# Performance work log

Hardware: AMD Instinct MI355X
Metric: run time of the kernel (lower is better)

Reference implementation:

```python
import jax, jax.numpy as jnp
import numpy as np


def setup_inputs() -> dict:
    key = jax.random.key(0)
    k1, k2, k3 = jax.random.split(key, 3)
    T, B, D, H = 256, 64, 1024, 2048
    sigma = 0.01
    inputs = jax.random.normal(k1, (T, B, D), dtype=jnp.float32)
    state = jnp.zeros((B, H), dtype=jnp.float32)
    W_xh = jax.random.uniform(k2, (D, H), dtype=jnp.float32) * sigma
    W_hh = jax.random.uniform(k3, (H, H), dtype=jnp.float32) * sigma
    b_h = jnp.zeros((H,), dtype=jnp.float32)
    return {"inputs": inputs, "state": state, "W_xh": W_xh, "W_hh": W_hh, "b_h": b_h}


def reference(inputs, state, W_xh, W_hh, b_h):
    # Precompute input projection for all steps in one big GEMM: [T,B,H]
    x_proj = jnp.einsum('tbd,dh->tbh', inputs, W_xh) + b_h

    def step(h, xp):
        h = jnp.tanh(h @ W_hh + xp)
        return h, h

    final_state, outputs = jax.lax.scan(step, state, x_proj)
    # outputs: [T, B, H] (stacked per-step hidden states), final_state: [B, H]
    return outputs, final_state
```

## Files before the change

### kernel.cpp

```cpp
#include <hip/hip_runtime.h>
#include <hip/hip_bf16.h>

#define T_STEPS 256
#define B_SZ    64
#define D_SZ    1024
#define H_SZ    2048
#define NBLK    256
#define TPB     320
#define HBUF    (B_SZ * H_SZ)

#define W_SCALE     256.0f
#define W_INV_SCALE 0.00390625f

typedef __attribute__((ext_vector_type(8))) _Float16 f16x8;
typedef __attribute__((ext_vector_type(4))) float    f32x4;


__global__ void cvt_f32_f16(const float* __restrict__ in,
                            _Float16* __restrict__ out, int n, float scale) {
    int i = blockIdx.x * blockDim.x + threadIdx.x;
    if (i < n) out[i] = (_Float16)(in[i] * scale);
}

__global__ void transpose_to_f16(const float* __restrict__ in,
                                 _Float16* __restrict__ out,
                                 int rows, int log2cols, float scale) {
    int i = blockIdx.x * blockDim.x + threadIdx.x;
    int cols = 1 << log2cols;
    if (i >= rows * cols) return;
    int r = i >> log2cols;
    int c = i & (cols - 1);
    out[c * rows + r] = (_Float16)(in[i] * scale);
}

__global__ void init_ctrs(unsigned int* ctr) {
    ctr[threadIdx.x + blockIdx.x * blockDim.x] = 0u;
}

__global__ __launch_bounds__(256) void gemm_xproj(
    const _Float16* __restrict__ A,
    const _Float16* __restrict__ BT,
    const float* __restrict__ bias,
    float* __restrict__ C,
    int M, int N, int K)
{
    int wave = threadIdx.x >> 6;
    int lane = threadIdx.x & 63;
    int q = lane >> 4;
    int r = lane & 15;
    int m0 = blockIdx.x * 128 + (wave >> 1) * 64;
    int n0 = blockIdx.y * 128 + (wave & 1) * 64;

    f32x4 acc[4][4] = {};
    for (int k = 0; k < K; k += 32) {
        int kk = k + q * 8;
        f16x8 a[4], b[4];
#pragma unroll
        for (int i = 0; i < 4; i++)
            a[i] = *(const f16x8*)(A + (size_t)(m0 + i * 16 + r) * K + kk);
#pragma unroll
        for (int j = 0; j < 4; j++)
            b[j] = *(const f16x8*)(BT + (size_t)(n0 + j * 16 + r) * K + kk);
#pragma unroll
        for (int i = 0; i < 4; i++)
#pragma unroll
            for (int j = 0; j < 4; j++)
                acc[i][j] = __builtin_amdgcn_mfma_f32_16x16x32_f16(a[i], b[j], acc[i][j], 0, 0, 0);
    }
#pragma unroll
    for (int i = 0; i < 4; i++)
#pragma unroll
        for (int j = 0; j < 4; j++)
#pragma unroll
            for (int reg = 0; reg < 4; reg++) {
                int row = m0 + i * 16 + q * 4 + reg;
                int col = n0 + j * 16 + r;
                C[(size_t)row * N + col] = acc[i][j][reg] * W_INV_SCALE + bias[col];
            }
}

template<bool CHAIN>
__global__ __launch_bounds__(TPB, 1) void rnn_persist(
    _Float16* __restrict__ hbase,
    _Float16* __restrict__ hb1,
    const _Float16* __restrict__ WT,
    float* __restrict__ out,
    float* __restrict__ final_out,
    unsigned int* __restrict__ ctr)
{
    __shared__ f16x8 wfrag[8192];
    __shared__ float part[4][2][256];
    __shared__ __align__(16) _Float16 hsl[16 * 32];
    __shared__ int pdone[4];
    __shared__ int hdone1, go;

    int tid = threadIdx.x;
    int bid = blockIdx.x;
    int g   = (bid >> 1) & 3;
    int c   = ((bid >> 3) << 1) | (bid & 1);
    int n0  = c * 32;
    int row0 = g * 16;

    if (tid == 0) {
        pdone[0] = pdone[1] = pdone[2] = pdone[3] = 0;
        hdone1 = 0; go = 0;
    }

    for (int idx = tid; idx < 8192; idx += TPB) {
        int kb = idx >> 7, j = (idx >> 6) & 1, l = idx & 63;
        wfrag[idx] = *(const f16x8*)(WT + (size_t)(n0 + j * 16 + (l & 15)) * H_SZ
                                        + kb * 32 + (l >> 4) * 8);
    }
    __syncthreads();

    int wave = tid >> 6, lane = tid & 63;

    if (wave == 4) {
        float c0 = 1.0f + lane, c1 = 2.0f, c2 = 3.0f, c3 = 4.0f;
        const float k1 = 1.0000001f, k2 = 1.0e-30f;
        while (__hip_atomic_load(&go, __ATOMIC_RELAXED, __HIP_MEMORY_SCOPE_WORKGROUP) < T_STEPS) {
#pragma unroll
            for (int z = 0; z < 64; z++) {
                c0 = __builtin_fmaf(c0, k1, k2);
                c1 = __builtin_fmaf(c1, k1, k2);
                c2 = __builtin_fmaf(c2, k1, k2);
                c3 = __builtin_fmaf(c3, k1, k2);
            }
        }
        __asm__ volatile("" :: "v"(c0), "v"(c1), "v"(c2), "v"(c3));
        return;
    }

    int q = lane >> 4, r = lane & 15;
    unsigned int* aline = ctr + (g * 2 + (bid & 1)) * 32;

    float xp[4];
    if (wave < 2) {
#pragma unroll
        for (int s = 0; s < 4; s++)
            xp[s] = out[(size_t)(row0 + q + 4 * s) * H_SZ + n0 + wave * 16 + r];
    }

    for (int t = 0; t < T_STEPS; t++) {
        const _Float16* hp;
        _Float16*       hn;
        if constexpr (CHAIN) {
            hp = hbase + (size_t)t * HBUF;
            hn = hbase + (size_t)(t + 1) * HBUF;
        } else {
            hp = (t & 1) ? hb1 : hbase;
            hn = (t & 1) ? hbase : hb1;
        }
        float* out_t = out + (size_t)t * B_SZ * H_SZ;
        int tg = t + 1;

        const _Float16* arow = hp + (size_t)(row0 + r) * H_SZ + q * 8;
        f16x8 abuf[16];
#pragma unroll
        for (int p = 0; p < 16; p++) {
            if constexpr (CHAIN) {
                abuf[p] = *(const f16x8*)(arow + (wave * 16 + p) * 32);
            } else {
                union { unsigned long long u[2]; f16x8 v; } au;
                au.u[0] = __hip_atomic_load((unsigned long long*)(arow + (wave * 16 + p) * 32),
                                            __ATOMIC_RELAXED, __HIP_MEMORY_SCOPE_AGENT);
                au.u[1] = __hip_atomic_load((unsigned long long*)(arow + (wave * 16 + p) * 32) + 1,
                                            __ATOMIC_RELAXED, __HIP_MEMORY_SCOPE_AGENT);
                abuf[p] = au.v;
            }
        }
        f32x4 acc[2] = {};
#pragma unroll
        for (int p = 0; p < 16; p++) {
            int kb = wave * 16 + p;
            acc[0] = __builtin_amdgcn_mfma_f32_16x16x32_f16(abuf[p], wfrag[kb * 128 + lane],      acc[0], 0, 0, 0);
            acc[1] = __builtin_amdgcn_mfma_f32_16x16x32_f16(abuf[p], wfrag[kb * 128 + 64 + lane], acc[1], 0, 0, 0);
        }

#pragma unroll
        for (int h = 0; h < 2; h++)
            *(f32x4*)&part[wave][h][lane * 4] = acc[h];
        __asm__ volatile("s_waitcnt lgkmcnt(0)" ::: "memory");
        if (lane == 0)
            __hip_atomic_store(&pdone[wave], tg, __ATOMIC_RELAXED, __HIP_MEMORY_SCOPE_WORKGROUP);

        if (wave >= 2) {
            if (t == T_STEPS - 1) break;
            while (__hip_atomic_load(&go, __ATOMIC_RELAXED, __HIP_MEMORY_SCOPE_WORKGROUP) < tg) { }
            continue;
        }

        for (int w = 0; w < 4; w++)
            if (w != wave)
                while (__hip_atomic_load(&pdone[w], __ATOMIC_RELAXED, __HIP_MEMORY_SCOPE_WORKGROUP) < tg) { }
        __asm__ volatile("" ::: "memory");

        bool last = (t == T_STEPS - 1);
#pragma unroll
        for (int s = 0; s < 4; s++) {
            int row = q + 4 * s;
            int idx = (s * 16 + r) * 4 + q;
            float sum = part[0][wave][idx] + part[1][wave][idx]
                      + part[2][wave][idx] + part[3][wave][idx];
            float v = tanhf(sum * W_INV_SCALE + xp[s]);
            size_t o = (size_t)(row0 + row) * H_SZ + n0 + wave * 16 + r;
            out_t[o] = v;
            if (last) final_out[o] = v;
            hsl[row * 32 + wave * 16 + r] = (_Float16)v;
        }
        if (last) {
            if (wave == 0 && lane == 0)
                __hip_atomic_store(&go, T_STEPS, __ATOMIC_RELAXED, __HIP_MEMORY_SCOPE_WORKGROUP);
            break;
        }

        const float* out_t1 = out_t + B_SZ * H_SZ;
#pragma unroll
        for (int s = 0; s < 4; s++)
            xp[s] = out_t1[(size_t)(row0 + q + 4 * s) * H_SZ + n0 + wave * 16 + r];

        __asm__ volatile("s_waitcnt lgkmcnt(0)" ::: "memory");
        {
            int rl = lane >> 2, pi = wave * 4 + (lane & 3);
            unsigned long long vv = ((const unsigned long long*)hsl)[rl * 8 + pi];
            __hip_atomic_store((unsigned long long*)(hn + (size_t)(row0 + rl) * H_SZ + n0) + pi,
                               vv, __ATOMIC_RELAXED, __HIP_MEMORY_SCOPE_AGENT);
        }
        __builtin_amdgcn_s_waitcnt(0);

        if (wave == 1) {
            if (lane == 0)
                __hip_atomic_store(&hdone1, tg, __ATOMIC_RELAXED, __HIP_MEMORY_SCOPE_WORKGROUP);
            while (__hip_atomic_load(&go, __ATOMIC_RELAXED, __HIP_MEMORY_SCOPE_WORKGROUP) < tg) { }
            continue;
        }
        while (__hip_atomic_load(&hdone1, __ATOMIC_RELAXED, __HIP_MEMORY_SCOPE_WORKGROUP) < tg) { }
        if (lane == 0)
            __hip_atomic_fetch_add(aline, 1u, __ATOMIC_RELAXED, __HIP_MEMORY_SCOPE_AGENT);
        unsigned int line_tgt = (unsigned int)tg * 32u;
        for (;;) {
            unsigned int v = __hip_atomic_load(ctr + (g * 2 + (lane & 1)) * 32,
                                               __ATOMIC_RELAXED, __HIP_MEMORY_SCOPE_AGENT);
            if (__ballot(v < line_tgt) == 0ull) break;
        }
        if (lane == 0)
            __hip_atomic_store(&go, tg, __ATOMIC_RELAXED, __HIP_MEMORY_SCOPE_WORKGROUP);
    }
}


extern "C" void kernel_launch(void* const* d_in, const int* in_sizes, int n_in,
                              void* d_out, int out_size, void* d_ws, size_t ws_size,
                              hipStream_t stream) {
    const float* inputs = (const float*)d_in[0];
    const float* state  = (const float*)d_in[1];
    const float* W_xh   = (const float*)d_in[2];
    const float* W_hh   = (const float*)d_in[3];
    const float* b_h    = (const float*)d_in[4];
    float* out = (float*)d_out;
    char* ws = (char*)d_ws;

    const size_t MB = 1ull << 20;
    const size_t OFF_WXT   = 0;
    const size_t OFF_WHT   = 4 * MB;
    const size_t OFF_CTR   = 12 * MB;
    const size_t OFF_CHAIN = 12 * MB + 8192;
    const size_t NEED_CHAIN = OFF_CHAIN + (size_t)(T_STEPS + 1) * HBUF * 2;

    const size_t F_IN  = 0;
    const size_t F_WXT = F_IN  + (size_t)T_STEPS * B_SZ * D_SZ * 2;
    const size_t F_WHT = F_WXT + (size_t)H_SZ * D_SZ * 2;
    const size_t F_H0  = F_WHT + (size_t)H_SZ * H_SZ * 2;
    const size_t F_H1  = F_H0  + (size_t)HBUF * 2;
    const size_t F_CTR = F_H1  + (size_t)HBUF * 2;
    const size_t NEED_PP = F_CTR + 4096;

    const int n_in_el = T_STEPS * B_SZ * D_SZ;
    dim3 g1((T_STEPS * B_SZ) / 128, H_SZ / 128);
    float* final_out = out + (size_t)T_STEPS * B_SZ * H_SZ;

    if (ws_size >= NEED_CHAIN) {
        _Float16* WxT    = (_Float16*)(ws + OFF_WXT);
        _Float16* WhT    = (_Float16*)(ws + OFF_WHT);
        unsigned int* ctr = (unsigned int*)(ws + OFF_CTR);
        _Float16* hchain = (_Float16*)(ws + OFF_CHAIN);
        _Float16* inputs_f16 = hchain + HBUF;
        _Float16* hb1 = nullptr;

        cvt_f32_f16<<<(n_in_el + 255) / 256, 256, 0, stream>>>(inputs, inputs_f16, n_in_el, 1.0f);
        transpose_to_f16<<<(D_SZ * H_SZ + 255) / 256, 256, 0, stream>>>(W_xh, WxT, D_SZ, 11, W_SCALE);
        transpose_to_f16<<<(H_SZ * H_SZ + 255) / 256, 256, 0, stream>>>(W_hh, WhT, H_SZ, 11, W_SCALE);
        cvt_f32_f16<<<(B_SZ * H_SZ + 255) / 256, 256, 0, stream>>>(state, hchain, B_SZ * H_SZ, 1.0f);
        init_ctrs<<<4, 256, 0, stream>>>(ctr);

        gemm_xproj<<<g1, 256, 0, stream>>>(inputs_f16, WxT, b_h, out,
                                           T_STEPS * B_SZ, H_SZ, D_SZ);

        void* args[] = { (void*)&hchain, (void*)&hb1, (void*)&WhT,
                         (void*)&out, (void*)&final_out, (void*)&ctr };
        hipLaunchCooperativeKernel((void*)rnn_persist<true>, dim3(NBLK), dim3(TPB),
                                   args, 0, stream);
    } else {
        if (ws_size < NEED_PP) return;
        _Float16* inputs_f16 = (_Float16*)(ws + F_IN);
        _Float16* WxT    = (_Float16*)(ws + F_WXT);
        _Float16* WhT    = (_Float16*)(ws + F_WHT);
        _Float16* hbuf0  = (_Float16*)(ws + F_H0);
        _Float16* hbuf1  = (_Float16*)(ws + F_H1);
        unsigned int* ctr = (unsigned int*)(ws + F_CTR);

        cvt_f32_f16<<<(n_in_el + 255) / 256, 256, 0, stream>>>(inputs, inputs_f16, n_in_el, 1.0f);
        transpose_to_f16<<<(D_SZ * H_SZ + 255) / 256, 256, 0, stream>>>(W_xh, WxT, D_SZ, 11, W_SCALE);
        transpose_to_f16<<<(H_SZ * H_SZ + 255) / 256, 256, 0, stream>>>(W_hh, WhT, H_SZ, 11, W_SCALE);
        cvt_f32_f16<<<(B_SZ * H_SZ + 255) / 256, 256, 0, stream>>>(state, hbuf0, B_SZ * H_SZ, 1.0f);
        init_ctrs<<<4, 256, 0, stream>>>(ctr);

        gemm_xproj<<<g1, 256, 0, stream>>>(inputs_f16, WxT, b_h, out,
                                           T_STEPS * B_SZ, H_SZ, D_SZ);

        void* args[] = { (void*)&hbuf0, (void*)&hbuf1, (void*)&WhT,
                         (void*)&out, (void*)&final_out, (void*)&ctr };
        hipLaunchCooperativeKernel((void*)rnn_persist<false>, dim3(NBLK), dim3(TPB),
                                   args, 0, stream);
    }
}
```

Before: 1.816 ms.

## Fuse input projection into persistent RNN kernel via a producer wave

Adds a sixth wave per block that computes each step's input projection slice with MFMA directly from fp16 inputs and W_xh. It writes the slice into double-buffered shared memory, and the tanh waves wait on a flag for it. This removes the separate large x-projection GEMM and its fp32 round trip through the output buffer, overlapping that work with the recurrence. The conversion kernels are also vectorised, and the weight transposes now use a shared-memory tile for coalescing. The cost is that the producer wave's global loads can add latency to the serial step chain if it falls behind.

```diff
diff --git a/kernel.cpp b/kernel.cpp
--- a/kernel.cpp
+++ b/kernel.cpp
@@ -6,31 +6,42 @@
 #define D_SZ    1024
 #define H_SZ    2048
 #define NBLK    256
-#define TPB     320
+#define TPB_F   384
+#define TPB_NF  320
 #define HBUF    (B_SZ * H_SZ)
 
 #define W_SCALE     256.0f
 #define W_INV_SCALE 0.00390625f
 
 typedef __attribute__((ext_vector_type(8))) _Float16 f16x8;
+typedef __attribute__((ext_vector_type(4))) _Float16 f16x4;
 typedef __attribute__((ext_vector_type(4))) float    f32x4;
 
 
 __global__ void cvt_f32_f16(const float* __restrict__ in,
-                            _Float16* __restrict__ out, int n, float scale) {
+                            _Float16* __restrict__ out, int n4, float scale) {
     int i = blockIdx.x * blockDim.x + threadIdx.x;
-    if (i < n) out[i] = (_Float16)(in[i] * scale);
+    if (i < n4) {
+        float4 v = ((const float4*)in)[i];
+        f16x4 o = { (_Float16)(v.x * scale), (_Float16)(v.y * scale),
+                    (_Float16)(v.z * scale), (_Float16)(v.w * scale) };
+        ((f16x4*)out)[i] = o;
+    }
 }
 
 __global__ void transpose_to_f16(const float* __restrict__ in,
                                  _Float16* __restrict__ out,
-                                 int rows, int log2cols, float scale) {
-    int i = blockIdx.x * blockDim.x + threadIdx.x;
-    int cols = 1 << log2cols;
-    if (i >= rows * cols) return;
-    int r = i >> log2cols;
-    int c = i & (cols - 1);
-    out[c * rows + r] = (_Float16)(in[i] * scale);
+                                 int rows, int cols, float scale) {
+    __shared__ float tile[32][33];
+    int tx = threadIdx.x & 31, ty = threadIdx.x >> 5;
+    int r0 = blockIdx.y * 32, c0 = blockIdx.x * 32;
+#pragma unroll
+    for (int i = 0; i < 32; i += 8)
+        tile[ty + i][tx] = in[(size_t)(r0 + ty + i) * cols + c0 + tx];
+    __syncthreads();
+#pragma unroll
+    for (int i = 0; i < 32; i += 8)
+        out[(size_t)(c0 + ty + i) * rows + r0 + tx] = (_Float16)(tile[tx][ty + i] * scale);
 }
 
 __global__ void init_ctrs(unsigned int* ctr) {
@@ -79,20 +90,25 @@
             }
 }
 
-template<bool CHAIN>
-__global__ __launch_bounds__(TPB, 1) void rnn_persist(
+template<bool CHAIN, bool FUSED>
+__global__ __launch_bounds__(TPB_F, 1) void rnn_persist(
     _Float16* __restrict__ hbase,
     _Float16* __restrict__ hb1,
     const _Float16* __restrict__ WT,
+    const _Float16* __restrict__ xin,
+    const _Float16* __restrict__ WxT,
+    const float*    __restrict__ bias,
     float* __restrict__ out,
     float* __restrict__ final_out,
     unsigned int* __restrict__ ctr)
 {
+    constexpr int NT = FUSED ? TPB_F : TPB_NF;
     __shared__ f16x8 wfrag[8192];
     __shared__ float part[4][2][256];
     __shared__ __align__(16) _Float16 hsl[16 * 32];
+    __shared__ float xpl[2][16][32];
     __shared__ int pdone[4];
-    __shared__ int hdone1, go;
+    __shared__ int hdone1, go, xpready;
 
     int tid = threadIdx.x;
     int bid = blockIdx.x;
@@ -103,10 +119,10 @@
 
     if (tid == 0) {
         pdone[0] = pdone[1] = pdone[2] = pdone[3] = 0;
-        hdone1 = 0; go = 0;
-    }
-
-    for (int idx = tid; idx < 8192; idx += TPB) {
+        hdone1 = 0; go = 0; xpready = 0;
+    }
+
+    for (int idx = tid; idx < 8192; idx += NT) {
         int kb = idx >> 7, j = (idx >> 6) & 1, l = idx & 63;
         wfrag[idx] = *(const f16x8*)(WT + (size_t)(n0 + j * 16 + (l & 15)) * H_SZ
                                         + kb * 32 + (l >> 4) * 8);
@@ -131,14 +147,56 @@
         return;
     }
 
+    if constexpr (FUSED) {
+        if (wave == 5) {
+            int q = lane >> 4, r = lane & 15;
+            float bj0 = bias[n0 + r];
+            float bj1 = bias[n0 + 16 + r];
+            const _Float16* wr0 = WxT + (size_t)(n0 + r) * D_SZ + q * 8;
+            const _Float16* wr1 = WxT + (size_t)(n0 + 16 + r) * D_SZ + q * 8;
+            for (int t = 0; t < T_STEPS; t++) {
+                if (t >= 2)
+                    while (__hip_atomic_load(&go, __ATOMIC_RELAXED, __HIP_MEMORY_SCOPE_WORKGROUP) < t - 1) { }
+                const _Float16* xr = xin + ((size_t)t * B_SZ + row0 + r) * D_SZ + q * 8;
+                f32x4 xacc0 = {}, xacc1 = {};
+                for (int k = 0; k < D_SZ; k += 128) {
+                    f16x8 xa[4], xb0[4], xb1[4];
+#pragma unroll
+                    for (int p = 0; p < 4; p++) {
+                        xa[p]  = *(const f16x8*)(xr  + k + p * 32);
+                        xb0[p] = *(const f16x8*)(wr0 + k + p * 32);
+                        xb1[p] = *(const f16x8*)(wr1 + k + p * 32);
+                    }
+#pragma unroll
+                    for (int p = 0; p < 4; p++) {
+                        xacc0 = __builtin_amdgcn_mfma_f32_16x16x32_f16(xa[p], xb0[p], xacc0, 0, 0, 0);
+                        xacc1 = __builtin_amdgcn_mfma_f32_16x16x32_f16(xa[p], xb1[p], xacc1, 0, 0, 0);
+                    }
+                }
+                float* xs = &xpl[t & 1][0][0];
+#pragma unroll
+                for (int reg = 0; reg < 4; reg++) {
+                    xs[(q * 4 + reg) * 32 + r]      = xacc0[reg] * W_INV_SCALE + bj0;
+                    xs[(q * 4 + reg) * 32 + 16 + r] = xacc1[reg] * W_INV_SCALE + bj1;
+                }
+                __asm__ volatile("s_waitcnt lgkmcnt(0)" ::: "memory");
+                if (lane == 0)
+                    __hip_atomic_store(&xpready, t + 1, __ATOMIC_RELAXED, __HIP_MEMORY_SCOPE_WORKGROUP);
+            }
+            return;
+        }
+    }
+
     int q = lane >> 4, r = lane & 15;
     unsigned int* aline = ctr + (g * 2 + (bid & 1)) * 32;
 
-    float xp[4];
-    if (wave < 2) {
-#pragma unroll
-        for (int s = 0; s < 4; s++)
-            xp[s] = out[(size_t)(row0 + q + 4 * s) * H_SZ + n0 + wave * 16 + r];
+    float xp[4] = {0.f, 0.f, 0.f, 0.f};
+    if constexpr (!FUSED) {
+        if (wave < 2) {
+#pragma unroll
+            for (int s = 0; s < 4; s++)
+                xp[s] = out[(size_t)(row0 + q + 4 * s) * H_SZ + n0 + wave * 16 + r];
+        }
     }
 
     for (int t = 0; t < T_STEPS; t++) {
@@ -195,6 +253,11 @@
                 while (__hip_atomic_load(&pdone[w], __ATOMIC_RELAXED, __HIP_MEMORY_SCOPE_WORKGROUP) < tg) { }
         __asm__ volatile("" ::: "memory");
 
+        if constexpr (FUSED) {
+            while (__hip_atomic_load(&xpready, __ATOMIC_RELAXED, __HIP_MEMORY_SCOPE_WORKGROUP) < tg) { }
+            __asm__ volatile("" ::: "memory");
+        }
+
         bool last = (t == T_STEPS - 1);
 #pragma unroll
         for (int s = 0; s < 4; s++) {
@@ -202,7 +265,10 @@
             int idx = (s * 16 + r) * 4 + q;
             float sum = part[0][wave][idx] + part[1][wave][idx]
                       + part[2][wave][idx] + part[3][wave][idx];
-            float v = tanhf(sum * W_INV_SCALE + xp[s]);
+            float xv;
+            if constexpr (FUSED) xv = xpl[t & 1][row][wave * 16 + r];
+            else                 xv = xp[s];
+            float v = tanhf(sum * W_INV_SCALE + xv);
             size_t o = (size_t)(row0 + row) * H_SZ + n0 + wave * 16 + r;
             out_t[o] = v;
             if (last) final_out[o] = v;
@@ -214,10 +280,12 @@
             break;
         }
 
-        const float* out_t1 = out_t + B_SZ * H_SZ;
-#pragma unroll
-        for (int s = 0; s < 4; s++)
-            xp[s] = out_t1[(size_t)(row0 + q + 4 * s) * H_SZ + n0 + wave * 16 + r];
+        if constexpr (!FUSED) {
+            const float* out_t1 = out_t + B_SZ * H_SZ;
+#pragma unroll
+            for (int s = 0; s < 4; s++)
+                xp[s] = out_t1[(size_t)(row0 + q + 4 * s) * H_SZ + n0 + wave * 16 + r];
+        }
 
         __asm__ volatile("s_waitcnt lgkmcnt(0)" ::: "memory");
         {
@@ -261,14 +329,20 @@
     char* ws = (char*)d_ws;
 
     const size_t MB = 1ull << 20;
-    const size_t OFF_WXT   = 0;
-    const size_t OFF_WHT   = 4 * MB;
-    const size_t OFF_CTR   = 12 * MB;
-    const size_t OFF_CHAIN = 12 * MB + 8192;
+    const size_t XIN_BYTES = (size_t)T_STEPS * B_SZ * D_SZ * 2;
+
+    const size_t OFF_WXT     = 0;
+    const size_t OFF_WHT     = 4 * MB;
+    const size_t OFF_CTR     = 12 * MB;
+    const size_t OFF_XIN     = 12 * MB + 8192;
+    const size_t OFF_CHAIN_F = OFF_XIN + XIN_BYTES;
+    const size_t NEED_FUSED  = OFF_CHAIN_F + (size_t)(T_STEPS + 1) * HBUF * 2;
+
+    const size_t OFF_CHAIN  = 12 * MB + 8192;
     const size_t NEED_CHAIN = OFF_CHAIN + (size_t)(T_STEPS + 1) * HBUF * 2;
 
     const size_t F_IN  = 0;
-    const size_t F_WXT = F_IN  + (size_t)T_STEPS * B_SZ * D_SZ * 2;
+    const size_t F_WXT = F_IN  + XIN_BYTES;
     const size_t F_WHT = F_WXT + (size_t)H_SZ * D_SZ * 2;
     const size_t F_H0  = F_WHT + (size_t)H_SZ * H_SZ * 2;
     const size_t F_H1  = F_H0  + (size_t)HBUF * 2;
@@ -279,26 +353,54 @@
     dim3 g1((T_STEPS * B_SZ) / 128, H_SZ / 128);
     float* final_out = out + (size_t)T_STEPS * B_SZ * H_SZ;
 
-    if (ws_size >= NEED_CHAIN) {
-        _Float16* WxT    = (_Float16*)(ws + OFF_WXT);
-        _Float16* WhT    = (_Float16*)(ws + OFF_WHT);
+    if (ws_size >= NEED_FUSED) {
+        _Float16* WxT     = (_Float16*)(ws + OFF_WXT);
+        _Float16* WhT     = (_Float16*)(ws + OFF_WHT);
         unsigned int* ctr = (unsigned int*)(ws + OFF_CTR);
-        _Float16* hchain = (_Float16*)(ws + OFF_CHAIN);
+        _Float16* xin     = (_Float16*)(ws + OFF_XIN);
+        _Float16* hchain  = (_Float16*)(ws + OFF_CHAIN_F);
+        _Float16* hb1 = nullptr;
+
+        cvt_f32_f16<<<(n_in_el / 4 + 255) / 256, 256, 0, stream>>>(inputs, xin, n_in_el / 4, 1.0f);
+        transpose_to_f16<<<dim3(H_SZ / 32, D_SZ / 32), 256, 0, stream>>>(W_xh, WxT, D_SZ, H_SZ, W_SCALE);
+        transpose_to_f16<<<dim3(H_SZ / 32, H_SZ / 32), 256, 0, stream>>>(W_hh, WhT, H_SZ, H_SZ, W_SCALE);
+        cvt_f32_f16<<<(B_SZ * H_SZ / 4 + 255) / 256, 256, 0, stream>>>(state, hchain, B_SZ * H_SZ / 4, 1.0f);
+        init_ctrs<<<4, 256, 0, stream>>>(ctr);
+
+        const _Float16* WhT_c  = WhT;
+        const _Float16* xin_c  = xin;
+        const _Float16* WxT_c  = WxT;
+        const float*    bias_c = b_h;
+        void* args[] = { (void*)&hchain, (void*)&hb1, (void*)&WhT_c, (void*)&xin_c,
+                         (void*)&WxT_c, (void*)&bias_c, (void*)&out, (void*)&final_out,
+                         (void*)&ctr };
+        hipLaunchCooperativeKernel((void*)rnn_persist<true, true>, dim3(NBLK), dim3(TPB_F),
+                                   args, 0, stream);
+    } else if (ws_size >= NEED_CHAIN) {
+        _Float16* WxT     = (_Float16*)(ws + OFF_WXT);
+        _Float16* WhT     = (_Float16*)(ws + OFF_WHT);
+        unsigned int* ctr = (unsigned int*)(ws + OFF_CTR);
+        _Float16* hchain  = (_Float16*)(ws + OFF_CHAIN);
         _Float16* inputs_f16 = hchain + HBUF;
         _Float16* hb1 = nullptr;
 
-        cvt_f32_f16<<<(n_in_el + 255) / 256, 256, 0, stream>>>(inputs, inputs_f16, n_in_el, 1.0f);
-        transpose_to_f16<<<(D_SZ * H_SZ + 255) / 256, 256, 0, stream>>>(W_xh, WxT, D_SZ, 11, W_SCALE);
-        transpose_to_f16<<<(H_SZ * H_SZ + 255) / 256, 256, 0, stream>>>(W_hh, WhT, H_SZ, 11, W_SCALE);
-        cvt_f32_f16<<<(B_SZ * H_SZ + 255) / 256, 256, 0, stream>>>(state, hchain, B_SZ * H_SZ, 1.0f);
+        cvt_f32_f16<<<(n_in_el / 4 + 255) / 256, 256, 0, stream>>>(inputs, inputs_f16, n_in_el / 4, 1.0f);
+        transpose_to_f16<<<dim3(H_SZ / 32, D_SZ / 32), 256, 0, stream>>>(W_xh, WxT, D_SZ, H_SZ, W_SCALE);
+        transpose_to_f16<<<dim3(H_SZ / 32, H_SZ / 32), 256, 0, stream>>>(W_hh, WhT, H_SZ, H_SZ, W_SCALE);
+        cvt_f32_f16<<<(B_SZ * H_SZ / 4 + 255) / 256, 256, 0, stream>>>(state, hchain, B_SZ * H_SZ / 4, 1.0f);
         init_ctrs<<<4, 256, 0, stream>>>(ctr);
 
         gemm_xproj<<<g1, 256, 0, stream>>>(inputs_f16, WxT, b_h, out,
                                            T_STEPS * B_SZ, H_SZ, D_SZ);
 
-        void* args[] = { (void*)&hchain, (void*)&hb1, (void*)&WhT,
-                         (void*)&out, (void*)&final_out, (void*)&ctr };
-        hipLaunchCooperativeKernel((void*)rnn_persist<true>, dim3(NBLK), dim3(TPB),
+        const _Float16* WhT_c  = WhT;
+        const _Float16* xin_c  = nullptr;
+        const _Float16* WxT_c  = nullptr;
+        const float*    bias_c = nullptr;
+        void* args[] = { (void*)&hchain, (void*)&hb1, (void*)&WhT_c, (void*)&xin_c,
+                         (void*)&WxT_c, (void*)&bias_c, (void*)&out, (void*)&final_out,
+                         (void*)&ctr };
+        hipLaunchCooperativeKernel((void*)rnn_persist<true, false>, dim3(NBLK), dim3(TPB_NF),
                                    args, 0, stream);
     } else {
         if (ws_size < NEED_PP) return;
@@ -309,18 +411,23 @@
         _Float16* hbuf1  = (_Float16*)(ws + F_H1);
         unsigned int* ctr = (unsigned int*)(ws + F_CTR);
 
-        cvt_f32_f16<<<(n_in_el + 255) / 256, 256, 0, stream>>>(inputs, inputs_f16, n_in_el, 1.0f);
-        transpose_to_f16<<<(D_SZ * H_SZ + 255) / 256, 256, 0, stream>>>(W_xh, WxT, D_SZ, 11, W_SCALE);
-        transpose_to_f16<<<(H_SZ * H_SZ + 255) / 256, 256, 0, stream>>>(W_hh, WhT, H_SZ, 11, W_SCALE);
-        cvt_f32_f16<<<(B_SZ * H_SZ + 255) / 256, 256, 0, stream>>>(state, hbuf0, B_SZ * H_SZ, 1.0f);
+        cvt_f32_f16<<<(n_in_el / 4 + 255) / 256, 256, 0, stream>>>(inputs, inputs_f16, n_in_el / 4, 1.0f);
+        transpose_to_f16<<<dim3(H_SZ / 32, D_SZ / 32), 256, 0, stream>>>(W_xh, WxT, D_SZ, H_SZ, W_SCALE);
+        transpose_to_f16<<<dim3(H_SZ / 32, H_SZ / 32), 256, 0, stream>>>(W_hh, WhT, H_SZ, H_SZ, W_SCALE);
+        cvt_f32_f16<<<(B_SZ * H_SZ / 4 + 255) / 256, 256, 0, stream>>>(state, hbuf0, B_SZ * H_SZ / 4, 1.0f);
         init_ctrs<<<4, 256, 0, stream>>>(ctr);
 
         gemm_xproj<<<g1, 256, 0, stream>>>(inputs_f16, WxT, b_h, out,
                                            T_STEPS * B_SZ, H_SZ, D_SZ);
 
-        void* args[] = { (void*)&hbuf0, (void*)&hbuf1, (void*)&WhT,
-                         (void*)&out, (void*)&final_out, (void*)&ctr };
-        hipLaunchCooperativeKernel((void*)rnn_persist<false>, dim3(NBLK), dim3(TPB),
+        const _Float16* WhT_c  = WhT;
+        const _Float16* xin_c  = nullptr;
+        const _Float16* WxT_c  = nullptr;
+        const float*    bias_c = nullptr;
+        void* args[] = { (void*)&hbuf0, (void*)&hbuf1, (void*)&WhT_c, (void*)&xin_c,
+                         (void*)&WxT_c, (void*)&bias_c, (void*)&out, (void*)&final_out,
+                         (void*)&ctr };
+        hipLaunchCooperativeKernel((void*)rnn_persist<false, false>, dim3(NBLK), dim3(TPB_NF),
                                    args, 0, stream);
     }
 }
```

Result: slower. 2.405 ms (+32.4%).

## Vectorize conversion, tile transposes through LDS, stage GEMM operands via global_load_lds

Applied to the files above, without the earlier changes.

The f32→f16 conversion kernel now handles four elements per thread with float4 loads. The weight transposes use a 32x32 shared-memory tile so that both reads and writes are coalesced. The input-projection GEMM now stages its A and B tiles into LDS with direct global-to-LDS loads and block barriers, instead of each wave reading global memory on its own. These changes target the preprocessing and x-projection phases. The persistent recurrent kernel, likely the dominant cost, is unchanged, and the GEMM adds a barrier per K-step with no double buffering.

```diff
diff --git a/kernel.cpp b/kernel.cpp
--- a/kernel.cpp
+++ b/kernel.cpp
@@ -13,28 +13,44 @@
 #define W_INV_SCALE 0.00390625f
 
 typedef __attribute__((ext_vector_type(8))) _Float16 f16x8;
+typedef __attribute__((ext_vector_type(4))) _Float16 f16x4;
 typedef __attribute__((ext_vector_type(4))) float    f32x4;
 
 
 __global__ void cvt_f32_f16(const float* __restrict__ in,
-                            _Float16* __restrict__ out, int n, float scale) {
+                            _Float16* __restrict__ out, int n4, float scale) {
     int i = blockIdx.x * blockDim.x + threadIdx.x;
-    if (i < n) out[i] = (_Float16)(in[i] * scale);
+    if (i < n4) {
+        float4 v = ((const float4*)in)[i];
+        f16x4 o = { (_Float16)(v.x * scale), (_Float16)(v.y * scale),
+                    (_Float16)(v.z * scale), (_Float16)(v.w * scale) };
+        ((f16x4*)out)[i] = o;
+    }
 }
 
 __global__ void transpose_to_f16(const float* __restrict__ in,
                                  _Float16* __restrict__ out,
-                                 int rows, int log2cols, float scale) {
-    int i = blockIdx.x * blockDim.x + threadIdx.x;
-    int cols = 1 << log2cols;
-    if (i >= rows * cols) return;
-    int r = i >> log2cols;
-    int c = i & (cols - 1);
-    out[c * rows + r] = (_Float16)(in[i] * scale);
+                                 int rows, int cols, float scale) {
+    __shared__ float tile[32][33];
+    int tx = threadIdx.x & 31, ty = threadIdx.x >> 5;
+    int r0 = blockIdx.y * 32, c0 = blockIdx.x * 32;
+#pragma unroll
+    for (int i = 0; i < 32; i += 8)
+        tile[ty + i][tx] = in[(size_t)(r0 + ty + i) * cols + c0 + tx];
+    __syncthreads();
+#pragma unroll
+    for (int i = 0; i < 32; i += 8)
+        out[(size_t)(c0 + ty + i) * rows + r0 + tx] = (_Float16)(tile[tx][ty + i] * scale);
 }
 
 __global__ void init_ctrs(unsigned int* ctr) {
     ctr[threadIdx.x + blockIdx.x * blockDim.x] = 0u;
+}
+
+#define GBK 32
+__device__ __forceinline__ void gload_lds16(const _Float16* g, _Float16* l) {
+    __builtin_amdgcn_global_load_lds((const __attribute__((address_space(1))) void*)g,
+                                     (__attribute__((address_space(3))) void*)l, 16, 0, 0);
 }
 
 __global__ __launch_bounds__(256) void gemm_xproj(
@@ -44,28 +60,47 @@
     float* __restrict__ C,
     int M, int N, int K)
 {
-    int wave = threadIdx.x >> 6;
-    int lane = threadIdx.x & 63;
+    __shared__ _Float16 As[128 * GBK];
+    __shared__ _Float16 Bs[128 * GBK];
+
+    int tid  = threadIdx.x;
+    int wave = tid >> 6;
+    int lane = tid & 63;
     int q = lane >> 4;
     int r = lane & 15;
-    int m0 = blockIdx.x * 128 + (wave >> 1) * 64;
-    int n0 = blockIdx.y * 128 + (wave & 1) * 64;
+    int m0 = blockIdx.x * 128;
+    int n0 = blockIdx.y * 128;
+    int wr = (wave >> 1) * 64;
+    int wc = (wave & 1) * 64;
+
+    int srow  = lane >> 2;
+    int skoff = (lane & 3) * 8;
 
     f32x4 acc[4][4] = {};
-    for (int k = 0; k < K; k += 32) {
-        int kk = k + q * 8;
+    for (int k0 = 0; k0 < K; k0 += GBK) {
+#pragma unroll
+        for (int i = 0; i < 2; i++) {
+            int chunk = wave * 2 + i;
+            int row = chunk * 16 + srow;
+            gload_lds16(A  + (size_t)(m0 + row) * K + k0 + skoff, As + chunk * 512);
+            gload_lds16(BT + (size_t)(n0 + row) * K + k0 + skoff, Bs + chunk * 512);
+        }
+        __asm__ volatile("s_waitcnt vmcnt(0)" ::: "memory");
+        __syncthreads();
+
         f16x8 a[4], b[4];
 #pragma unroll
         for (int i = 0; i < 4; i++)
-            a[i] = *(const f16x8*)(A + (size_t)(m0 + i * 16 + r) * K + kk);
+            a[i] = *(const f16x8*)(As + (wr + i * 16 + r) * GBK + q * 8);
 #pragma unroll
         for (int j = 0; j < 4; j++)
-            b[j] = *(const f16x8*)(BT + (size_t)(n0 + j * 16 + r) * K + kk);
+            b[j] = *(const f16x8*)(Bs + (wc + j * 16 + r) * GBK + q * 8);
 #pragma unroll
         for (int i = 0; i < 4; i++)
 #pragma unroll
             for (int j = 0; j < 4; j++)
                 acc[i][j] = __builtin_amdgcn_mfma_f32_16x16x32_f16(a[i], b[j], acc[i][j], 0, 0, 0);
+        __syncthreads();
     }
 #pragma unroll
     for (int i = 0; i < 4; i++)
@@ -73,8 +108,8 @@
         for (int j = 0; j < 4; j++)
 #pragma unroll
             for (int reg = 0; reg < 4; reg++) {
-                int row = m0 + i * 16 + q * 4 + reg;
-                int col = n0 + j * 16 + r;
+                int row = m0 + wr + i * 16 + q * 4 + reg;
+                int col = n0 + wc + j * 16 + r;
                 C[(size_t)row * N + col] = acc[i][j][reg] * W_INV_SCALE + bias[col];
             }
 }
@@ -287,10 +322,10 @@
         _Float16* inputs_f16 = hchain + HBUF;
         _Float16* hb1 = nullptr;
 
-        cvt_f32_f16<<<(n_in_el + 255) / 256, 256, 0, stream>>>(inputs, inputs_f16, n_in_el, 1.0f);
-        transpose_to_f16<<<(D_SZ * H_SZ + 255) / 256, 256, 0, stream>>>(W_xh, WxT, D_SZ, 11, W_SCALE);
-        transpose_to_f16<<<(H_SZ * H_SZ + 255) / 256, 256, 0, stream>>>(W_hh, WhT, H_SZ, 11, W_SCALE);
-        cvt_f32_f16<<<(B_SZ * H_SZ + 255) / 256, 256, 0, stream>>>(state, hchain, B_SZ * H_SZ, 1.0f);
+        cvt_f32_f16<<<(n_in_el / 4 + 255) / 256, 256, 0, stream>>>(inputs, inputs_f16, n_in_el / 4, 1.0f);
+        transpose_to_f16<<<dim3(H_SZ / 32, D_SZ / 32), 256, 0, stream>>>(W_xh, WxT, D_SZ, H_SZ, W_SCALE);
+        transpose_to_f16<<<dim3(H_SZ / 32, H_SZ / 32), 256, 0, stream>>>(W_hh, WhT, H_SZ, H_SZ, W_SCALE);
+        cvt_f32_f16<<<(B_SZ * H_SZ / 4 + 255) / 256, 256, 0, stream>>>(state, hchain, B_SZ * H_SZ / 4, 1.0f);
         init_ctrs<<<4, 256, 0, stream>>>(ctr);
 
         gemm_xproj<<<g1, 256, 0, stream>>>(inputs_f16, WxT, b_h, out,
@@ -309,10 +344,10 @@
         _Float16* hbuf1  = (_Float16*)(ws + F_H1);
         unsigned int* ctr = (unsigned int*)(ws + F_CTR);
 
-        cvt_f32_f16<<<(n_in_el + 255) / 256, 256, 0, stream>>>(inputs, inputs_f16, n_in_el, 1.0f);
-        transpose_to_f16<<<(D_SZ * H_SZ + 255) / 256, 256, 0, stream>>>(W_xh, WxT, D_SZ, 11, W_SCALE);
-        transpose_to_f16<<<(H_SZ * H_SZ + 255) / 256, 256, 0, stream>>>(W_hh, WhT, H_SZ, 11, W_SCALE);
-        cvt_f32_f16<<<(B_SZ * H_SZ + 255) / 256, 256, 0, stream>>>(state, hbuf0, B_SZ * H_SZ, 1.0f);
+        cvt_f32_f16<<<(n_in_el / 4 + 255) / 256, 256, 0, stream>>>(inputs, inputs_f16, n_in_el / 4, 1.0f);
+        transpose_to_f16<<<dim3(H_SZ / 32, D_SZ / 32), 256, 0, stream>>>(W_xh, WxT, D_SZ, H_SZ, W_SCALE);
+        transpose_to_f16<<<dim3(H_SZ / 32, H_SZ / 32), 256, 0, stream>>>(W_hh, WhT, H_SZ, H_SZ, W_SCALE);
+        cvt_f32_f16<<<(B_SZ * H_SZ / 4 + 255) / 256, 256, 0, stream>>>(state, hbuf0, B_SZ * H_SZ / 4, 1.0f);
         init_ctrs<<<4, 256, 0, stream>>>(ctr);
 
         gemm_xproj<<<g1, 256, 0, stream>>>(inputs_f16, WxT, b_h, out,
```

Result: faster. 1.654 ms (-8.9%).
